# Kernel optimization log

Hardware: AMD Instinct MI355X
Metric: run time of the kernel (lower is better)

Reference implementation:

```python
import jax, jax.numpy as jnp
import numpy as np
import math

B, E, N = 32, 256, 64
KV_DIM, Q_DIM = 100, 768


def setup_inputs() -> dict:
    key = jax.random.key(0)
    ks = jax.random.split(key, 8)
    q = jax.random.normal(ks[0], (B, Q_DIM), dtype=jnp.float32)
    k = jax.random.normal(ks[1], (B, E, N, KV_DIM), dtype=jnp.float32)
    v = jax.random.normal(ks[2], (B, E, N, KV_DIM), dtype=jnp.float32)
    input_ent = jax.random.randint(ks[3], (B, E), 0, 50000)
    # xavier-uniform-initialized weights (torch Linear: y = x @ W.T + b)
    def xavier(k_, fan_out, fan_in):
        lim = math.sqrt(6.0 / (fan_in + fan_out))
        return jax.random.uniform(k_, (fan_out, fan_in), jnp.float32, -lim, lim)
    W_q = xavier(ks[4], KV_DIM, Q_DIM)
    b_q = jnp.zeros((KV_DIM,), jnp.float32)
    W_kv = xavier(ks[5], KV_DIM, KV_DIM)
    W_v = xavier(ks[6], KV_DIM, KV_DIM)
    return {"input_ent": input_ent, "q": q, "k": k, "v": v,
            "W_q": W_q, "b_q": b_q, "W_kv": W_kv, "W_v": W_v}


def reference(input_ent, q, k, v, W_q, b_q, W_kv, W_v):
    # mode == 'candidate_pos', graphsage=False -> output = self_attention(q, k, v)
    # Q projection + tanh: [B, Kv]
    Qp = jnp.tanh(q @ W_q.T + b_q)
    # K projection: [B, E, N, Kv]
    Kp = k @ W_kv.T
    # broadcasted dot-product score: [B, E, N]
    att = jnp.einsum('bd,bend->ben', Qp, Kp) / math.sqrt(KV_DIM)
    # masked_fill(att == 0, -10000)
    att = jnp.where(att == 0.0, jnp.float32(-10000.0), att)
    # LeakyReLU (default negative_slope=0.01) then softmax over neighbor dim
    att = jax.nn.softmax(jax.nn.leaky_relu(att, 0.01), axis=2)
    # masked_fill(att == 1/N, 0)
    att = jnp.where(att == jnp.float32(1.0 / N), jnp.float32(0.0), att)
    # V projection and weighted aggregation over neighbors: [B, E, Kv]
    Vp = v @ W_v.T
    return jnp.einsum('ben,bend->bed', att, Vp)
```

## Files before the change

kernel.cpp:

```cpp
#include <hip/hip_runtime.h>

#define B 32
#define E 256
#define N 64
#define KV 100
#define QD 768
#define NF4 ((N * KV) / 4)
#define WF4 ((KV * KV) / 4)

__device__ __forceinline__ float dot4(float4 a, float4 b) {
    return a.x * b.x + a.y * b.y + a.z * b.z + a.w * b.w;
}

#define ASYNC16(gsrc, ldst) \
    __builtin_amdgcn_global_load_lds( \
        (const __attribute__((address_space(1))) void*)(gsrc), \
        (__attribute__((address_space(3))) void*)(ldst), 16, 0, 0)

__global__ __launch_bounds__(256) void prep_kernel(
    const float* __restrict__ q,
    const float* __restrict__ W_q,
    const float* __restrict__ b_q,
    const float* __restrict__ W_kv,
    float* __restrict__ Qk)
{
    const int tid = threadIdx.x;
    const int b   = blockIdx.x;

    __shared__ float q_lds[QD];
    __shared__ float Qp_lds[KV];

    for (int i = tid; i < QD; i += 256) q_lds[i] = q[b * QD + i];
    __syncthreads();

    const int i = tid >> 1, h = tid & 1;
    if (i < KV) {
        float acc = 0.f;
        const float* wrow = W_q + i * QD + h * (QD / 2);
        const float* qrow = q_lds + h * (QD / 2);
        #pragma unroll 8
        for (int d = 0; d < QD / 2; d++) acc += qrow[d] * wrow[d];
        acc += __shfl_xor(acc, 1);
        if (h == 0) Qp_lds[i] = tanhf(acc + b_q[i]);
    }
    __syncthreads();

    if (tid < KV) {
        float acc = 0.f;
        #pragma unroll 4
        for (int ii = 0; ii < KV; ii++) acc += Qp_lds[ii] * W_kv[ii * KV + tid];
        Qk[b * KV + tid] = acc * 0.1f;
    }
}

__global__ __launch_bounds__(256, 4) void attn_kernel(
    const float* __restrict__ k,
    const float* __restrict__ v,
    const float* __restrict__ Qk,
    const float* __restrict__ W_v,
    float* __restrict__ out)
{
    __shared__ __align__(16) float vbuf[N * KV];
    __shared__ float kpbuf[NF4];
    __shared__ __align__(16) float qk_lds[4][KV];
    __shared__ float att_lds[N];
    __shared__ __align__(16) float agg_lds[KV];

    const int tid  = threadIdx.x;
    const int wid  = tid >> 6;
    const int lane = tid & 63;
    const int be   = blockIdx.x;
    const int b    = be >> 8;

    const float4* kb4 = (const float4*)(k + (size_t)be * (N * KV));
    const float4* vb4 = (const float4*)(v + (size_t)be * (N * KV));
    float4* vbuf4 = (float4*)vbuf;

    float4 qkreg = make_float4(0.f, 0.f, 0.f, 0.f);
    if (lane < KV / 4) qkreg = ((const float4*)(Qk + b * KV))[lane];

    float4 kk[7];
    #pragma unroll
    for (int r = 0; r < 7; r++) {
        int f = r * 256 + tid;
        kk[r] = (f < NF4) ? kb4[f] : make_float4(0.f, 0.f, 0.f, 0.f);
    }

    #pragma unroll
    for (int i = 0; i < 6; i++)
        ASYNC16(vb4 + i * 256 + tid, vbuf4 + i * 256 + (tid & 192));
    if (tid < 64) ASYNC16(vb4 + 1536 + tid, vbuf4 + 1536);

    if (lane < KV / 4) ((float4*)qk_lds[wid])[lane] = qkreg;

    int c = tid % 25;
    const int c0 = c;
    #pragma unroll
    for (int r = 0; r < 7; r++) {
        int f = r * 256 + tid;
        if (f < NF4) {
            float4 qq = ((const float4*)qk_lds[wid])[c];
            kpbuf[f] = dot4(kk[r], qq);
        }
        c += 6; if (c >= 25) c -= 25;
    }
    __syncthreads();

    if (tid < N) {
        float s = 0.f;
        #pragma unroll
        for (int j = 0; j < 25; j++) s += kpbuf[tid * 25 + j];
        if (s == 0.0f) s = -10000.0f;
        s = (s > 0.0f) ? s : 0.01f * s;
        float m = s;
        #pragma unroll
        for (int o = 32; o; o >>= 1) m = fmaxf(m, __shfl_xor(m, o));
        float e = __expf(s - m);
        float su = e;
        #pragma unroll
        for (int o = 32; o; o >>= 1) su += __shfl_xor(su, o);
        float r = e / su;
        if (r == 0.015625f) r = 0.f;
        att_lds[tid] = r;
    }
    __syncthreads();

    if (tid < KV) {
        float a = 0.f;
        #pragma unroll 8
        for (int n = 0; n < N; n++)
            a += att_lds[n] * vbuf[n * KV + tid];
        agg_lds[tid] = a;
    }
    __syncthreads();

    {
        const float4* wv4g = (const float4*)W_v;
        float4 wv[10];
        #pragma unroll
        for (int r = 0; r < 10; r++) {
            int f = r * 256 + tid;
            wv[r] = (f < WF4) ? wv4g[f] : make_float4(0.f, 0.f, 0.f, 0.f);
        }
        c = c0;
        #pragma unroll
        for (int r = 0; r < 10; r++) {
            int f = r * 256 + tid;
            if (f < WF4) {
                float4 a = ((const float4*)agg_lds)[c];
                vbuf[f] = dot4(wv[r], a);
            }
            c += 6; if (c >= 25) c -= 25;
        }
    }
    __syncthreads();

    if (tid < KV) {
        float s = 0.f;
        #pragma unroll
        for (int j = 0; j < 25; j++) s += vbuf[tid * 25 + j];
        out[(size_t)be * KV + tid] = s;
    }
}

extern "C" void kernel_launch(void* const* d_in, const int* in_sizes, int n_in,
                              void* d_out, int out_size, void* d_ws, size_t ws_size,
                              hipStream_t stream) {
    const float* q    = (const float*)d_in[1];
    const float* k    = (const float*)d_in[2];
    const float* v    = (const float*)d_in[3];
    const float* W_q  = (const float*)d_in[4];
    const float* b_q  = (const float*)d_in[5];
    const float* W_kv = (const float*)d_in[6];
    const float* W_v  = (const float*)d_in[7];
    float* out  = (float*)d_out;

    float* Qk = (float*)d_ws;

    prep_kernel<<<B, 256, 0, stream>>>(q, W_q, b_q, W_kv, Qk);
    attn_kernel<<<B * E, 256, 0, stream>>>(k, v, Qk, W_v, out);
}
```

Measured before the change: 104.9 us.

## Split W_v projection into separate kernel and use nontemporal loads for K

```diff
diff --git a/kernel.cpp b/kernel.cpp
--- a/kernel.cpp
+++ b/kernel.cpp
@@ -6,22 +6,26 @@
 #define KV 100
 #define QD 768
 #define NF4 ((N * KV) / 4)
-#define WF4 ((KV * KV) / 4)
 
-__device__ __forceinline__ float dot4(float4 a, float4 b) {
-    return a.x * b.x + a.y * b.y + a.z * b.z + a.w * b.w;
-}
+typedef float floatx4 __attribute__((ext_vector_type(4)));
 
 #define ASYNC16(gsrc, ldst) \
     __builtin_amdgcn_global_load_lds( \
         (const __attribute__((address_space(1))) void*)(gsrc), \
         (__attribute__((address_space(3))) void*)(ldst), 16, 0, 0)
 
+__device__ __forceinline__ float dot4f(float4 a, float4 b) {
+    return a.x * b.x + a.y * b.y + a.z * b.z + a.w * b.w;
+}
+
+__device__ __forceinline__ float4 ntload4(const float4* p) {
+    floatx4 r = __builtin_nontemporal_load((const floatx4*)p);
+    return make_float4(r.x, r.y, r.z, r.w);
+}
+
 __global__ __launch_bounds__(256) void prep_kernel(
-    const float* __restrict__ q,
-    const float* __restrict__ W_q,
-    const float* __restrict__ b_q,
-    const float* __restrict__ W_kv,
+    const float* __restrict__ q, const float* __restrict__ W_q,
+    const float* __restrict__ b_q, const float* __restrict__ W_kv,
     float* __restrict__ Qk)
 {
     const int tid = threadIdx.x;
@@ -57,14 +61,12 @@
     const float* __restrict__ k,
     const float* __restrict__ v,
     const float* __restrict__ Qk,
-    const float* __restrict__ W_v,
-    float* __restrict__ out)
+    float* __restrict__ agg_out)
 {
     __shared__ __align__(16) float vbuf[N * KV];
     __shared__ float kpbuf[NF4];
     __shared__ __align__(16) float qk_lds[4][KV];
     __shared__ float att_lds[N];
-    __shared__ __align__(16) float agg_lds[KV];
 
     const int tid  = threadIdx.x;
     const int wid  = tid >> 6;
@@ -82,8 +84,8 @@
     float4 kk[7];
     #pragma unroll
     for (int r = 0; r < 7; r++) {
-        int f = r * 256 + tid;
-        kk[r] = (f < NF4) ? kb4[f] : make_float4(0.f, 0.f, 0.f, 0.f);
+        int f = r * 256 + tid; if (f > NF4 - 1) f = NF4 - 1;
+        kk[r] = ntload4(kb4 + f);
     }
 
     #pragma unroll
@@ -94,13 +96,12 @@
     if (lane < KV / 4) ((float4*)qk_lds[wid])[lane] = qkreg;
 
     int c = tid % 25;
-    const int c0 = c;
     #pragma unroll
     for (int r = 0; r < 7; r++) {
         int f = r * 256 + tid;
         if (f < NF4) {
             float4 qq = ((const float4*)qk_lds[wid])[c];
-            kpbuf[f] = dot4(kk[r], qq);
+            kpbuf[f] = dot4f(kk[r], qq);
         }
         c += 6; if (c >= 25) c -= 25;
     }
@@ -130,36 +131,33 @@
         #pragma unroll 8
         for (int n = 0; n < N; n++)
             a += att_lds[n] * vbuf[n * KV + tid];
-        agg_lds[tid] = a;
+        agg_out[(size_t)be * KV + tid] = a;
     }
-    __syncthreads();
+}
 
-    {
-        const float4* wv4g = (const float4*)W_v;
-        float4 wv[10];
-        #pragma unroll
-        for (int r = 0; r < 10; r++) {
-            int f = r * 256 + tid;
-            wv[r] = (f < WF4) ? wv4g[f] : make_float4(0.f, 0.f, 0.f, 0.f);
+__global__ __launch_bounds__(256) void proj_kernel(
+    const float* __restrict__ agg,
+    const float* __restrict__ W_v,
+    float* __restrict__ out)
+{
+    __shared__ __align__(16) float a_lds[4][KV];
+    const int tid = threadIdx.x, wid = tid >> 6, lane = tid & 63;
+    const int be  = blockIdx.x * 4 + wid;
+
+    if (lane < 25)
+        ((float4*)a_lds[wid])[lane] = ((const float4*)(agg + (size_t)be * KV))[lane];
+
+    const float4* wv4 = (const float4*)W_v;
+    const float4* a4  = (const float4*)a_lds[wid];
+    #pragma unroll
+    for (int p = 0; p < 2; p++) {
+        const int i = p * 64 + lane;
+        if (i < KV) {
+            float acc = 0.f;
+            #pragma unroll
+            for (int j = 0; j < 25; j++) acc += dot4f(wv4[i * 25 + j], a4[j]);
+            out[(size_t)be * KV + i] = acc;
         }
-        c = c0;
-        #pragma unroll
-        for (int r = 0; r < 10; r++) {
-            int f = r * 256 + tid;
-            if (f < WF4) {
-                float4 a = ((const float4*)agg_lds)[c];
-                vbuf[f] = dot4(wv[r], a);
-            }
-            c += 6; if (c >= 25) c -= 25;
-        }
-    }
-    __syncthreads();
-
-    if (tid < KV) {
-        float s = 0.f;
-        #pragma unroll
-        for (int j = 0; j < 25; j++) s += vbuf[tid * 25 + j];
-        out[(size_t)be * KV + tid] = s;
     }
 }
 
@@ -175,8 +173,10 @@
     const float* W_v  = (const float*)d_in[7];
     float* out  = (float*)d_out;
 
-    float* Qk = (float*)d_ws;
+    float* Qk  = (float*)d_ws;
+    float* agg = Qk + B * KV;
 
     prep_kernel<<<B, 256, 0, stream>>>(q, W_q, b_q, W_kv, Qk);
-    attn_kernel<<<B * E, 256, 0, stream>>>(k, v, Qk, W_v, out);
+    attn_kernel<<<B * E, 256, 0, stream>>>(k, v, Qk, agg);
+    proj_kernel<<<(B * E) / 4, 256, 0, stream>>>(agg, W_v, out);
 }
```

After: 109.2 us. 4.1% more time.
